# Optimization experiments

Hardware: AMD Instinct MI355X
Metric: run time of the kernel (lower is better)

The kernel has to match this reference:

```python
import jax, jax.numpy as jnp
import numpy as np

EMBED = 256
HEADS = 8
HEAD_DIM = 32
MLP_DIM = 1024
NEG = -1e9  # large negative in place of -inf so fully-deselected rows don't NaN
LN_EPS = 1e-5


def _layernorm(x, g, b):
    m = jnp.mean(x, axis=-1, keepdims=True)
    v = jnp.mean(jnp.square(x - m), axis=-1, keepdims=True)
    return (x - m) / jnp.sqrt(v + LN_EPS) * g + b


def setup_inputs() -> dict:
    key = jax.random.key(0)
    ks = jax.random.split(key, 16)
    b, s, d = 64, 360, EMBED
    sc = 0.02
    return {
        "x": jax.random.normal(ks[0], (b, s, d), dtype=jnp.float32),
        "attention_mask": jnp.zeros((b, 1, 1, s), dtype=jnp.float32),
        # TokenRouter.weight_predictor: Linear(256, 1)
        "wp_w": jax.random.normal(ks[1], (1, d), dtype=jnp.float32) * sc,
        "wp_b": jnp.zeros((1,), dtype=jnp.float32),
        # TokenRouter.aux_predictor: Linear(256,128) -> SiLU -> Linear(128,2)
        "a1_w": jax.random.normal(ks[2], (d // 2, d), dtype=jnp.float32) * sc,
        "a1_b": jnp.zeros((d // 2,), dtype=jnp.float32),
        "a2_w": jax.random.normal(ks[3], (2, d // 2), dtype=jnp.float32) * sc,
        "a2_b": jnp.zeros((2,), dtype=jnp.float32),
        # transformer block (pre-LN GPT2-style)
        "ln1_g": jnp.ones((d,), dtype=jnp.float32),
        "ln1_b": jnp.zeros((d,), dtype=jnp.float32),
        "wqkv": jax.random.normal(ks[4], (d, 3 * d), dtype=jnp.float32) * sc,
        "bqkv": jnp.zeros((3 * d,), dtype=jnp.float32),
        "wo": jax.random.normal(ks[5], (d, d), dtype=jnp.float32) * sc,
        "bo": jnp.zeros((d,), dtype=jnp.float32),
        "ln2_g": jnp.ones((d,), dtype=jnp.float32),
        "ln2_b": jnp.zeros((d,), dtype=jnp.float32),
        "w1": jax.random.normal(ks[6], (d, MLP_DIM), dtype=jnp.float32) * sc,
        "b1": jnp.zeros((MLP_DIM,), dtype=jnp.float32),
        "w2": jax.random.normal(ks[7], (MLP_DIM, d), dtype=jnp.float32) * sc,
        "b2": jnp.zeros((d,), dtype=jnp.float32),
    }


def reference(x, attention_mask, wp_w, wp_b, a1_w, a1_b, a2_w, a2_b,
              ln1_g, ln1_b, wqkv, bqkv, wo, bo, ln2_g, ln2_b, w1, b1, w2, b2):
    b, s, d = x.shape
    # --- router: per-token scalar weight ---
    weights = (x @ wp_w.T + wp_b).squeeze(-1)  # [b, s]
    # --- aux predictor selects tokens (eval path: argmax over 2 logits) ---
    h = jax.nn.silu(x @ a1_w.T + a1_b)
    aux_logits = h @ a2_w.T + a2_b            # [b, s, 2]
    sel = jnp.argmax(aux_logits, axis=-1).astype(bool)  # [b, s]
    # --- masked transformer block over the selected token subset.
    # Compacting tokens then attending == full-seq attention with deselected
    # keys masked out (LN/MLP/residual are position-wise), so vectorize:
    bias = attention_mask + jnp.where(sel, 0.0, NEG)[:, None, None, :]  # [b,1,1,s]
    hn = _layernorm(x, ln1_g, ln1_b)
    qkv = hn @ wqkv + bqkv
    q, k, v = jnp.split(qkv, 3, axis=-1)
    q = q.reshape(b, s, HEADS, HEAD_DIM)
    k = k.reshape(b, s, HEADS, HEAD_DIM)
    v = v.reshape(b, s, HEADS, HEAD_DIM)
    scores = jnp.einsum("bqhd,bkhd->bhqk", q, k) / np.sqrt(HEAD_DIM).astype(np.float32)
    scores = scores + bias                   # [b, h, s, s]
    attn = jax.nn.softmax(scores, axis=-1)
    ctx = jnp.einsum("bhqk,bkhd->bqhd", attn, v).reshape(b, s, d)
    h1 = x + (ctx @ wo + bo)
    h2n = _layernorm(h1, ln2_g, ln2_b)
    block_out = h1 + (jax.nn.gelu(h2n @ w1 + b1) @ w2 + b2)  # [b, s, d]
    # --- scatter-recombine: selected -> weighted block output, else passthrough
    out = jnp.where(sel[..., None], block_out * weights[..., None], x)
    avg_selected = jnp.sum(sel.astype(x.dtype)) / b
    return out, avg_selected
```

## Files before the change

kernel.cpp:

```cpp
#include <hip/hip_runtime.h>
#include <math.h>
#include <stdint.h>

#define TOKN 23040
#define BSZ 64
#define SEQ 360
#define DIM 256
#define NHD 8
#define HDD 32
#define MLPD 1024
#define NEGV -1e9f

typedef __attribute__((ext_vector_type(8))) short bf16x8;
typedef __attribute__((ext_vector_type(4))) float f32x4;

static __device__ __forceinline__ short f2bs(float f) {
  unsigned u = __builtin_bit_cast(unsigned, f);
  u += 0x7fffu + ((u >> 16) & 1u);
  return (short)(u >> 16);
}
static __device__ __forceinline__ float bf2f(short s) {
  unsigned u = ((unsigned)(unsigned short)s) << 16;
  return __builtin_bit_cast(float, u);
}
static __device__ __forceinline__ unsigned packbf(float a, float b) {
  return (unsigned)(unsigned short)f2bs(a) | ((unsigned)(unsigned short)f2bs(b) << 16);
}
static __device__ __forceinline__ void gl16(const short* g, short* l) {
  __builtin_amdgcn_global_load_lds(
      (const __attribute__((address_space(1))) unsigned int*)g,
      (__attribute__((address_space(3))) unsigned int*)l, 16, 0, 0);
}

__global__ __launch_bounds__(256) void mega_k(
    const float* __restrict__ x, const float* __restrict__ g,
    const float* __restrict__ b, const float* __restrict__ wpw,
    const float* __restrict__ wpb, short* __restrict__ outn,
    float* __restrict__ wout, float* __restrict__ outx,
    const float* __restrict__ a1w, const float* __restrict__ a1b,
    const float* __restrict__ a2w, const float* __restrict__ a2b,
    int* __restrict__ sel,
    const float* __restrict__ wqkv, const float* __restrict__ wo,
    const float* __restrict__ w1, const float* __restrict__ w2,
    short* __restrict__ wqkvt, short* __restrict__ wot,
    short* __restrict__ w1t, short* __restrict__ w2t) {
  __shared__ __align__(16) unsigned char smem[49152];
  int bid = blockIdx.x;
  int t = threadIdx.x;

  if (bid < 180) {
    float(*XT)[192] = (float(*)[192])smem;
    float(*WT)[192] = (float(*)[192])(smem + 24576);
    int m0 = bid * 128;
    int tx = t & 15;
    int tyy = t >> 4;
    float acc[8][8] = {};
    int rs = t >> 1, cs = (t & 1) * 16;
    int scol = (rs >> 3) * 12 + (rs & 7);
    const float* xpb = x + (size_t)(m0 + rs) * 256 + cs;
    const float* wpb_ = a1w + (size_t)rs * 256 + cs;
    for (int k0 = 0; k0 < 256; k0 += 32) {
#pragma unroll
      for (int j4 = 0; j4 < 4; j4++) {
        float4 xv4 = *(const float4*)(xpb + k0 + j4 * 4);
        float4 wv4 = *(const float4*)(wpb_ + k0 + j4 * 4);
        XT[cs + j4 * 4 + 0][scol] = xv4.x;
        XT[cs + j4 * 4 + 1][scol] = xv4.y;
        XT[cs + j4 * 4 + 2][scol] = xv4.z;
        XT[cs + j4 * 4 + 3][scol] = xv4.w;
        WT[cs + j4 * 4 + 0][scol] = wv4.x;
        WT[cs + j4 * 4 + 1][scol] = wv4.y;
        WT[cs + j4 * 4 + 2][scol] = wv4.z;
        WT[cs + j4 * 4 + 3][scol] = wv4.w;
      }
      __syncthreads();
#pragma unroll 4
      for (int kk = 0; kk < 32; kk++) {
        float4 xa = *(const float4*)&XT[kk][tyy * 12];
        float4 xb = *(const float4*)&XT[kk][tyy * 12 + 4];
        float4 wa = *(const float4*)&WT[kk][tx * 12];
        float4 wb = *(const float4*)&WT[kk][tx * 12 + 4];
        float xr[8] = {xa.x, xa.y, xa.z, xa.w, xb.x, xb.y, xb.z, xb.w};
        float wr[8] = {wa.x, wa.y, wa.z, wa.w, wb.x, wb.y, wb.z, wb.w};
#pragma unroll
        for (int i = 0; i < 8; i++)
#pragma unroll
          for (int j = 0; j < 8; j++) acc[i][j] += xr[i] * wr[j];
      }
      __syncthreads();
    }
    float b1v[8], a20[8], a21[8];
#pragma unroll
    for (int j = 0; j < 8; j++) {
      int dim = tx * 8 + j;
      b1v[j] = a1b[dim];
      a20[j] = a2w[dim];
      a21[j] = a2w[128 + dim];
    }
    float bias0 = a2b[0], bias1 = a2b[1];
#pragma unroll
    for (int i = 0; i < 8; i++) {
      float l0 = 0.f, l1 = 0.f;
#pragma unroll
      for (int j = 0; j < 8; j++) {
        float v = acc[i][j] + b1v[j];
        float h = v / (1.f + expf(-v));
        l0 += h * a20[j];
        l1 += h * a21[j];
      }
#pragma unroll
      for (int o = 1; o < 16; o <<= 1) { l0 += __shfl_xor(l0, o); l1 += __shfl_xor(l1, o); }
      if (tx == 0) sel[m0 + tyy * 8 + i] = (l1 + bias1 > l0 + bias0) ? 1 : 0;
    }
  } else if (bid < 948) {
    float(*tile)[33] = (float(*)[33])smem;
    int b2 = bid - 180;
    const float* src;
    short* dst;
    int K, N, kt, nt;
    if (b2 < 192) {
      src = wqkv; dst = wqkvt; K = 256; N = 768; kt = b2 / 24; nt = b2 % 24;
    } else if (b2 < 256) {
      int bb = b2 - 192; src = wo; dst = wot; K = 256; N = 256; kt = bb >> 3; nt = bb & 7;
    } else if (b2 < 512) {
      int bb = b2 - 256; src = w1; dst = w1t; K = 256; N = 1024; kt = bb >> 5; nt = bb & 31;
    } else {
      int bb = b2 - 512; src = w2; dst = w2t; K = 1024; N = 256; kt = bb >> 3; nt = bb & 7;
    }
    int r = t >> 3, c4 = (t & 7) * 4;
    const float4 v = *(const float4*)(src + (size_t)(kt * 32 + r) * N + nt * 32 + c4);
    tile[c4 + 0][r] = v.x;
    tile[c4 + 1][r] = v.y;
    tile[c4 + 2][r] = v.z;
    tile[c4 + 3][r] = v.w;
    __syncthreads();
    union { short s[4]; uint2 u; } o;
    o.s[0] = f2bs(tile[r][c4 + 0]);
    o.s[1] = f2bs(tile[r][c4 + 1]);
    o.s[2] = f2bs(tile[r][c4 + 2]);
    o.s[3] = f2bs(tile[r][c4 + 3]);
    *(uint2*)(dst + (size_t)(nt * 32 + r) * K + kt * 32 + c4) = o.u;
  } else {
    int tok = (bid - 948) * 4 + (t >> 6);
    int lane = t & 63;
    const float4 xv = *(const float4*)(x + (size_t)tok * DIM + lane * 4);
    *(float4*)(outx + (size_t)tok * DIM + lane * 4) = xv;
    float s = xv.x + xv.y + xv.z + xv.w;
    float s2 = xv.x * xv.x + xv.y * xv.y + xv.z * xv.z + xv.w * xv.w;
#pragma unroll
    for (int o = 1; o < 64; o <<= 1) { s += __shfl_xor(s, o); s2 += __shfl_xor(s2, o); }
    float m = s * (1.f / DIM);
    float var = fmaxf(s2 * (1.f / DIM) - m * m, 0.f);
    float rstd = rsqrtf(var + 1e-5f);
    float4 gv = *(const float4*)(g + lane * 4);
    float4 bv = *(const float4*)(b + lane * 4);
    uint2 pk;
    pk.x = packbf((xv.x - m) * rstd * gv.x + bv.x, (xv.y - m) * rstd * gv.y + bv.y);
    pk.y = packbf((xv.z - m) * rstd * gv.z + bv.z, (xv.w - m) * rstd * gv.w + bv.w);
    *(uint2*)(outn + (size_t)tok * DIM + lane * 4) = pk;
    float4 wv = *(const float4*)(wpw + lane * 4);
    float wd = xv.x * wv.x + xv.y * wv.y + xv.z * wv.z + xv.w * wv.w;
#pragma unroll
    for (int o = 1; o < 64; o <<= 1) wd += __shfl_xor(wd, o);
    if (lane == 0) wout[tok] = wd + wpb[0];
  }
}

__global__ __launch_bounds__(512) void scan_k(
    const int* __restrict__ sel, int* __restrict__ g_idx,
    int* __restrict__ startp, int* __restrict__ cntp,
    int* __restrict__ mtotp, float* __restrict__ outavg) {
  __shared__ int sc[512];
  __shared__ int red[8];
  int b = blockIdx.x, t = threadIdx.x;
  int lane = t & 63, wave = t >> 6;
  int part = 0;
  for (int i = t; i < b * SEQ; i += 512) part += sel[i];
#pragma unroll
  for (int o = 1; o < 64; o <<= 1) part += __shfl_xor(part, o);
  if (lane == 0) red[wave] = part;
  __syncthreads();
  int start = 0;
#pragma unroll
  for (int w = 0; w < 8; w++) start += red[w];
  __syncthreads();
  int flag = (t < SEQ) ? sel[b * SEQ + t] : 0;
  sc[t] = flag;
  __syncthreads();
  int val = flag;
  for (int off = 1; off < 512; off <<= 1) {
    int add = (t >= off) ? sc[t - off] : 0;
    __syncthreads();
    val += add;
    sc[t] = val;
    __syncthreads();
  }
  if (flag) g_idx[start + val - 1] = b * SEQ + t;
  if (t == 511) { startp[b] = start; cntp[b] = val; }
  if (b == 63) {
    int mt = start + sc[511];
    if (t == 0) { *mtotp = mt; outavg[0] = (float)mt / 64.0f; }
    int e = mt + 256;
    if (e > TOKN) e = TOKN;
    for (int i = mt + t; i < e; i += 512) g_idx[i] = 0;
  }
}

template <int MODE, int BN>
__global__ __launch_bounds__(256) void gemm128_k(
    const short* __restrict__ A, const short* __restrict__ Bt,
    const float* __restrict__ bias, const float* __restrict__ resf,
    const short* __restrict__ resb, const float* __restrict__ wgt,
    const int* __restrict__ g_idx, const int* __restrict__ mtotp,
    short* __restrict__ outb, float* __restrict__ outf, int Ndim, int Kdim) {
  int Mt = *mtotp;
  int m0 = blockIdx.y * 128;
  if (m0 >= Mt) return;
  __shared__ __align__(16) short As[2][128 * 32];
  __shared__ __align__(16) short Bs[2][BN * 32];
  constexpr int NJ = BN / 32;
  int n0 = blockIdx.x * BN;
  int t = threadIdx.x;
  int wave = t >> 6, lane = t & 63;
  int l15 = lane & 15, quad = lane >> 4;
  int wr = (wave >> 1) * 64, wc = (wave & 1) * (BN / 2);
  int r0 = t >> 2, c0 = (t & 3) * 8;
  long arA = (MODE == 0) ? g_idx[m0 + r0] : (m0 + r0);
  long arB = (MODE == 0) ? g_idx[m0 + 64 + r0] : (m0 + 64 + r0);
  const short* gA0 = A + arA * Kdim + c0;
  const short* gA1 = A + arB * Kdim + c0;
  const short* gB0 = Bt + (size_t)(n0 + r0) * Kdim + c0;
  const short* gB1 = Bt + (size_t)(n0 + 64 + r0) * Kdim + c0;
  int wbase = wave * 512;

  f32x4 acc[4][NJ];
#pragma unroll
  for (int i = 0; i < 4; i++)
#pragma unroll
    for (int j = 0; j < NJ; j++)
#pragma unroll
      for (int r = 0; r < 4; r++) acc[i][j][r] = 0.f;

  int nst = Kdim >> 5;
  gl16(gA0, As[0] + wbase);
  gl16(gA1, As[0] + 2048 + wbase);
  gl16(gB0, Bs[0] + wbase);
  if constexpr (BN == 128) gl16(gB1, Bs[0] + 2048 + wbase);
  __syncthreads();

  int buf = 0;
  for (int s = 0; s < nst; ++s) {
    if (s + 1 < nst) {
      int off = (s + 1) * 32;
      short* d = (buf ^ 1) ? &As[1][0] : &As[0][0];
      short* e = (buf ^ 1) ? &Bs[1][0] : &Bs[0][0];
      gl16(gA0 + off, d + wbase);
      gl16(gA1 + off, d + 2048 + wbase);
      gl16(gB0 + off, e + wbase);
      if constexpr (BN == 128) gl16(gB1 + off, e + 2048 + wbase);
    }
    const short* Ab = buf ? &As[1][0] : &As[0][0];
    const short* Bb = buf ? &Bs[1][0] : &Bs[0][0];
    bf16x8 af[4], bfr[NJ];
#pragma unroll
    for (int i = 0; i < 4; i++)
      af[i] = *(const bf16x8*)&Ab[(wr + i * 16 + l15) * 32 + quad * 8];
#pragma unroll
    for (int j = 0; j < NJ; j++)
      bfr[j] = *(const bf16x8*)&Bb[(wc + j * 16 + l15) * 32 + quad * 8];
#pragma unroll
    for (int i = 0; i < 4; i++)
#pragma unroll
      for (int j = 0; j < NJ; j++)
        acc[i][j] = __builtin_amdgcn_mfma_f32_16x16x32_bf16(af[i], bfr[j],
                                                            acc[i][j], 0, 0, 0);
    __syncthreads();
    buf ^= 1;
  }

#pragma unroll
  for (int i = 0; i < 4; i++) {
#pragma unroll
    for (int j = 0; j < NJ; j++) {
      int col = n0 + wc + j * 16 + l15;
      float bcol = bias[col];
#pragma unroll
      for (int r = 0; r < 4; r++) {
        int row = m0 + wr + i * 16 + quad * 4 + r;
        float v = acc[i][j][r] + bcol;
        size_t idx = (size_t)row * Ndim + col;
        if (MODE == 0) {
          outb[idx] = f2bs(v);
        } else if (MODE == 2) {
          float u = 0.7978845608028654f * (v + 0.044715f * v * v * v);
          float e = __expf(2.f * u);
          float th = 1.f - 2.f / (e + 1.f);
          outb[idx] = f2bs(0.5f * v * (1.f + th));
        } else {
          if (row < Mt) {
            int orig = g_idx[row];
            float o = (v + bf2f(resb[idx])) * wgt[orig];
            outf[(size_t)orig * 256 + col] = o;
          }
        }
      }
    }
  }
}

__global__ __launch_bounds__(256) void wo_ln_k(
    const short* __restrict__ A, const short* __restrict__ Bt,
    const float* __restrict__ bias, const float* __restrict__ resf,
    const float* __restrict__ g2, const float* __restrict__ b2,
    const int* __restrict__ g_idx, const int* __restrict__ mtotp,
    short* __restrict__ h1b, short* __restrict__ h2n) {
  int Mt = *mtotp;
  int m0 = blockIdx.x * 128;
  if (m0 >= Mt) return;
  __shared__ __align__(16) short As[2][128 * 32];
  __shared__ __align__(16) short Bs[2][256 * 32];
  __shared__ float ps[128][2], ps2[128][2];
  int t = threadIdx.x;
  int wave = t >> 6, lane = t & 63;
  int l15 = lane & 15, quad = lane >> 4;
  int wr = (wave >> 1) * 64, wc = (wave & 1) * 128;
  int r0 = t >> 2, c0 = (t & 3) * 8;
  const short* gA0 = A + (size_t)(m0 + r0) * 256 + c0;
  const short* gA1 = A + (size_t)(m0 + 64 + r0) * 256 + c0;
  const short* gB0 = Bt + (size_t)r0 * 256 + c0;
  int wbase = wave * 512;

  f32x4 acc[4][8];
#pragma unroll
  for (int i = 0; i < 4; i++)
#pragma unroll
    for (int j = 0; j < 8; j++)
#pragma unroll
      for (int r = 0; r < 4; r++) acc[i][j][r] = 0.f;

  gl16(gA0, As[0] + wbase);
  gl16(gA1, As[0] + 2048 + wbase);
#pragma unroll
  for (int q = 0; q < 4; q++) gl16(gB0 + (size_t)q * 64 * 256, Bs[0] + q * 2048 + wbase);
  __syncthreads();

  int buf = 0;
  for (int s = 0; s < 8; ++s) {
    if (s + 1 < 8) {
      int off = (s + 1) * 32;
      short* d = (buf ^ 1) ? &As[1][0] : &As[0][0];
      short* e = (buf ^ 1) ? &Bs[1][0] : &Bs[0][0];
      gl16(gA0 + off, d + wbase);
      gl16(gA1 + off, d + 2048 + wbase);
#pragma unroll
      for (int q = 0; q < 4; q++)
        gl16(gB0 + (size_t)q * 64 * 256 + off, e + q * 2048 + wbase);
    }
    const short* Ab = buf ? &As[1][0] : &As[0][0];
    const short* Bb = buf ? &Bs[1][0] : &Bs[0][0];
    bf16x8 af[4], bfr[8];
#pragma unroll
    for (int i = 0; i < 4; i++)
      af[i] = *(const bf16x8*)&Ab[(wr + i * 16 + l15) * 32 + quad * 8];
#pragma unroll
    for (int j = 0; j < 8; j++)
      bfr[j] = *(const bf16x8*)&Bb[(wc + j * 16 + l15) * 32 + quad * 8];
#pragma unroll
    for (int i = 0; i < 4; i++)
#pragma unroll
      for (int j = 0; j < 8; j++)
        acc[i][j] = __builtin_amdgcn_mfma_f32_16x16x32_bf16(af[i], bfr[j],
                                                            acc[i][j], 0, 0, 0);
    __syncthreads();
    buf ^= 1;
  }

  float bcol[8], gcol[8], bbcol[8];
#pragma unroll
  for (int j = 0; j < 8; j++) {
    int col = wc + j * 16 + l15;
    bcol[j] = bias[col];
    gcol[j] = g2[col];
    bbcol[j] = b2[col];
  }
  float s1v[4][4], s2v[4][4];
#pragma unroll
  for (int i = 0; i < 4; i++) {
#pragma unroll
    for (int r = 0; r < 4; r++) {
      int row = m0 + wr + i * 16 + quad * 4 + r;
      int orig = g_idx[row];
      const float* xr = resf + (size_t)orig * 256;
      float ls_ = 0.f, ls2_ = 0.f;
#pragma unroll
      for (int j = 0; j < 8; j++) {
        int col = wc + j * 16 + l15;
        float h1 = acc[i][j][r] + bcol[j] + xr[col];
        acc[i][j][r] = h1;
        h1b[(size_t)row * 256 + col] = f2bs(h1);
        ls_ += h1;
        ls2_ += h1 * h1;
      }
      s1v[i][r] = ls_;
      s2v[i][r] = ls2_;
    }
  }
#pragma unroll
  for (int i = 0; i < 4; i++)
#pragma unroll
    for (int r = 0; r < 4; r++) {
#pragma unroll
      for (int o = 1; o < 16; o <<= 1) {
        s1v[i][r] += __shfl_xor(s1v[i][r], o);
        s2v[i][r] += __shfl_xor(s2v[i][r], o);
      }
    }
  if (l15 == 0) {
#pragma unroll
    for (int i = 0; i < 4; i++)
#pragma unroll
      for (int r = 0; r < 4; r++) {
        int lr = wr + i * 16 + quad * 4 + r;
        ps[lr][wave & 1] = s1v[i][r];
        ps2[lr][wave & 1] = s2v[i][r];
      }
  }
  __syncthreads();
#pragma unroll
  for (int i = 0; i < 4; i++) {
#pragma unroll
    for (int r = 0; r < 4; r++) {
      int lr = wr + i * 16 + quad * 4 + r;
      float S = ps[lr][0] + ps[lr][1];
      float S2 = ps2[lr][0] + ps2[lr][1];
      float m = S * (1.f / 256.f);
      float var = fmaxf(S2 * (1.f / 256.f) - m * m, 0.f);
      float rstd = rsqrtf(var + 1e-5f);
      int row = m0 + lr;
#pragma unroll
      for (int j = 0; j < 8; j++) {
        int col = wc + j * 16 + l15;
        float h2 = (acc[i][j][r] - m) * rstd * gcol[j] + bbcol[j];
        h2n[(size_t)row * 256 + col] = f2bs(h2);
      }
    }
  }
}

__global__ __launch_bounds__(256) void attn_k(
    const short* __restrict__ qkv, const float* __restrict__ amask,
    const int* __restrict__ g_idx, const int* __restrict__ startp,
    const int* __restrict__ cntp, short* __restrict__ ctx) {
  __shared__ __align__(16) short VF[2 * 12 * 64 * 8];
  __shared__ __align__(16) float ls[384];
  int bh = blockIdx.x >> 1, qhalf = blockIdx.x & 1;
  int bb = bh >> 3, h = bh & 7;
  int t = threadIdx.x;
  int start = startp[bb], cnt = cntp[bb];
  size_t base = (size_t)start * 768;
  for (int i = t; i < 1536; i += 256) {
    int k = i >> 2, cg = (i & 3) * 8;
    union { int4 v; short s[8]; } u;
    if (k < cnt) {
      u.v = *(const int4*)(qkv + base + (size_t)k * 768 + 512 + h * 32 + cg);
    } else {
      u.v = make_int4(0, 0, 0, 0);
    }
    int c = k >> 5, qd = (k >> 3) & 3, j = k & 7;
#pragma unroll
    for (int jj = 0; jj < 8; jj++) {
      int d = cg + jj;
      VF[((((d >> 4) * 12 + c) * 64) + qd * 16 + (d & 15)) * 8 + j] = u.s[jj];
    }
  }
  for (int i = t; i < 384; i += 256)
    ls[i] = (i < cnt) ? amask[g_idx[start + i]] : 0.f;
  __syncthreads();

  int wave = t >> 6, lane = t & 63;
  int ql = lane & 15, quad = lane >> 4;
  int addr0 = (((quad & 1) * 2) * 16 + ql) * 4;
  int addr1 = addr0 + 64;
  bool hiq = quad >= 2;
  int nt = (cnt + 15) >> 4;
  int nc = (cnt + 31) >> 5;

  for (int qt = qhalf + 2 * wave; qt < nt; qt += 8) {
    int q0 = qt * 16, qrow = q0 + ql;
    bf16x8 qf;
#pragma unroll
    for (int j = 0; j < 8; j++) qf[j] = 0;
    if (qrow < cnt)
      qf = *(const bf16x8*)(qkv + base + (size_t)qrow * 768 + h * 32 + quad * 8);

    f32x4 o0, o1;
#pragma unroll
    for (int r = 0; r < 4; r++) { o0[r] = 0.f; o1[r] = 0.f; }
    float lsum = 0.f;

    for (int c = 0; c < nc; c++) {
      int keyA = c * 32 + ql;
      int keyB = keyA + 16;
      bf16x8 kfA, kfB;
#pragma unroll
      for (int j = 0; j < 8; j++) { kfA[j] = 0; kfB[j] = 0; }
      if (keyA < cnt)
        kfA = *(const bf16x8*)(qkv + base + (size_t)keyA * 768 + 256 + h * 32 + quad * 8);
      if (keyB < cnt)
        kfB = *(const bf16x8*)(qkv + base + (size_t)keyB * 768 + 256 + h * 32 + quad * 8);
      f32x4 sa, sb;
#pragma unroll
      for (int r = 0; r < 4; r++) { sa[r] = 0.f; sb[r] = 0.f; }
      sa = __builtin_amdgcn_mfma_f32_16x16x32_bf16(kfA, qf, sa, 0, 0, 0);
      sb = __builtin_amdgcn_mfma_f32_16x16x32_bf16(kfB, qf, sb, 0, 0, 0);
      int kbase = c * 32 + quad * 4;
      float4 la = *(const float4*)&ls[kbase];
      float4 lb = *(const float4*)&ls[kbase + 16];
      float ea0 = (kbase + 0 < cnt) ? __expf(sa[0] * 0.17677669529663687f + la.x) : 0.f;
      float ea1 = (kbase + 1 < cnt) ? __expf(sa[1] * 0.17677669529663687f + la.y) : 0.f;
      float ea2 = (kbase + 2 < cnt) ? __expf(sa[2] * 0.17677669529663687f + la.z) : 0.f;
      float ea3 = (kbase + 3 < cnt) ? __expf(sa[3] * 0.17677669529663687f + la.w) : 0.f;
      float eb0 = (kbase + 16 < cnt) ? __expf(sb[0] * 0.17677669529663687f + lb.x) : 0.f;
      float eb1 = (kbase + 17 < cnt) ? __expf(sb[1] * 0.17677669529663687f + lb.y) : 0.f;
      float eb2 = (kbase + 18 < cnt) ? __expf(sb[2] * 0.17677669529663687f + lb.z) : 0.f;
      float eb3 = (kbase + 19 < cnt) ? __expf(sb[3] * 0.17677669529663687f + lb.w) : 0.f;
      lsum += (ea0 + ea1) + (ea2 + ea3) + (eb0 + eb1) + (eb2 + eb3);
      unsigned pA0 = packbf(ea0, ea1), pA1 = packbf(ea2, ea3);
      unsigned pB0 = packbf(eb0, eb1), pB1 = packbf(eb2, eb3);
      int s00 = __builtin_amdgcn_ds_bpermute(addr0, (int)pA0);
      int s10 = __builtin_amdgcn_ds_bpermute(addr0, (int)pB0);
      int s01 = __builtin_amdgcn_ds_bpermute(addr0, (int)pA1);
      int s11 = __builtin_amdgcn_ds_bpermute(addr0, (int)pB1);
      int s02 = __builtin_amdgcn_ds_bpermute(addr1, (int)pA0);
      int s12 = __builtin_amdgcn_ds_bpermute(addr1, (int)pB0);
      int s03 = __builtin_amdgcn_ds_bpermute(addr1, (int)pA1);
      int s13 = __builtin_amdgcn_ds_bpermute(addr1, (int)pB1);
      union { int i[4]; bf16x8 v; } pf;
      pf.i[0] = hiq ? s10 : s00;
      pf.i[1] = hiq ? s11 : s01;
      pf.i[2] = hiq ? s12 : s02;
      pf.i[3] = hiq ? s13 : s03;
      bf16x8 v0 = *(const bf16x8*)&VF[(c * 64 + lane) * 8];
      bf16x8 v1 = *(const bf16x8*)&VF[((12 + c) * 64 + lane) * 8];
      o0 = __builtin_amdgcn_mfma_f32_16x16x32_bf16(v0, pf.v, o0, 0, 0, 0);
      o1 = __builtin_amdgcn_mfma_f32_16x16x32_bf16(v1, pf.v, o1, 0, 0, 0);
    }
    lsum += __shfl_xor(lsum, 16);
    lsum += __shfl_xor(lsum, 32);
    float inv = 1.f / lsum;

    if (qrow < cnt) {
      size_t cb = ((size_t)(start + qrow)) * 256 + h * 32;
      uint2 w0, w1;
      w0.x = packbf(o0[0] * inv, o0[1] * inv);
      w0.y = packbf(o0[2] * inv, o0[3] * inv);
      w1.x = packbf(o1[0] * inv, o1[1] * inv);
      w1.y = packbf(o1[2] * inv, o1[3] * inv);
      *(uint2*)(ctx + cb + quad * 4) = w0;
      *(uint2*)(ctx + cb + 16 + quad * 4) = w1;
    }
  }
}

extern "C" void kernel_launch(void* const* d_in, const int* in_sizes, int n_in,
                              void* d_out, int out_size, void* d_ws,
                              size_t ws_size, hipStream_t stream) {
  const float* x = (const float*)d_in[0];
  const float* amask = (const float*)d_in[1];
  const float* wp_w = (const float*)d_in[2];
  const float* wp_b = (const float*)d_in[3];
  const float* a1_w = (const float*)d_in[4];
  const float* a1_b = (const float*)d_in[5];
  const float* a2_w = (const float*)d_in[6];
  const float* a2_b = (const float*)d_in[7];
  const float* ln1_g = (const float*)d_in[8];
  const float* ln1_b = (const float*)d_in[9];
  const float* wqkv = (const float*)d_in[10];
  const float* bqkv = (const float*)d_in[11];
  const float* wo = (const float*)d_in[12];
  const float* bo = (const float*)d_in[13];
  const float* ln2_g = (const float*)d_in[14];
  const float* ln2_b = (const float*)d_in[15];
  const float* w1 = (const float*)d_in[16];
  const float* b1 = (const float*)d_in[17];
  const float* w2 = (const float*)d_in[18];
  const float* b2 = (const float*)d_in[19];
  float* out = (float*)d_out;

  uint8_t* p = (uint8_t*)d_ws;
  float* weightsv = (float*)p; p += (size_t)TOKN * 4;
  int* selv = (int*)p;         p += (size_t)TOKN * 4;
  int* idxlv = (int*)p;        p += (size_t)TOKN * 4;
  int* gidxv = (int*)p;        p += (size_t)TOKN * 4;
  int* cntv = (int*)p;         p += 64 * 4;
  int* startv = (int*)p;       p += 64 * 4;
  int* mtotv = (int*)p;        p += 64 * 4;
  short* wqkvt = (short*)p;    p += (size_t)768 * 256 * 2;
  short* wot = (short*)p;      p += (size_t)256 * 256 * 2;
  short* w1t = (short*)p;      p += (size_t)1024 * 256 * 2;
  short* w2t = (short*)p;      p += (size_t)256 * 1024 * 2;
  short* h1bv = (short*)p;     p += (size_t)TOKN * 256 * 2;
  short* h2nv = (short*)p;     p += (size_t)TOKN * 256 * 2;
  short* ctxv = (short*)p;     p += (size_t)TOKN * 256 * 2;
  uint8_t* R = p;
  short* xnv = (short*)R;
  short* qkvv = (short*)(R + (size_t)TOKN * 256 * 2);
  short* actv = (short*)R;
  (void)idxlv;

  mega_k<<<dim3(6708), dim3(256), 0, stream>>>(
      x, ln1_g, ln1_b, wp_w, wp_b, xnv, weightsv, out,
      a1_w, a1_b, a2_w, a2_b, selv,
      wqkv, wo, w1, w2, wqkvt, wot, w1t, w2t);
  scan_k<<<dim3(64), dim3(512), 0, stream>>>(selv, gidxv, startv, cntv, mtotv,
                                             out + (size_t)TOKN * 256);
  gemm128_k<0, 128><<<dim3(6, 180), dim3(256), 0, stream>>>(
      xnv, wqkvt, bqkv, nullptr, nullptr, nullptr, gidxv, mtotv, qkvv, nullptr,
      768, 256);
  attn_k<<<dim3(1024), dim3(256), 0, stream>>>(qkvv, amask, gidxv, startv, cntv, ctxv);
  wo_ln_k<<<dim3(180), dim3(256), 0, stream>>>(ctxv, wot, bo, x, ln2_g, ln2_b,
                                               gidxv, mtotv, h1bv, h2nv);
  gemm128_k<2, 128><<<dim3(8, 180), dim3(256), 0, stream>>>(
      h2nv, w1t, b1, nullptr, nullptr, nullptr, gidxv, mtotv, actv, nullptr,
      1024, 256);
  gemm128_k<3, 64><<<dim3(4, 180), dim3(256), 0, stream>>>(
      actv, w2t, b2, nullptr, h1bv, weightsv, gidxv, mtotv, nullptr, out, 256, 1024);
}
```

Measured before the change: 249.2 us.

## Shrink mega kernel blocks to 128 threads and retile router GEMM to 32 rows

Changes the fused prologue kernel from 256-thread to 128-thread blocks. The router GEMM now uses 32-token tiles (720 blocks instead of 180), each thread accumulating a 4x8 tile, and LDS use drops. The weight-transpose and LayerNorm sections are remapped to the smaller block. The aim is to fill more CUs with the router work, which previously ran on only 180 large blocks. In exchange, each block re-reads the full a1 weight matrix four times as often, and the block count roughly doubles.

```diff
diff --git a/kernel.cpp b/kernel.cpp
--- a/kernel.cpp
+++ b/kernel.cpp
@@ -32,7 +32,7 @@
       (__attribute__((address_space(3))) unsigned int*)l, 16, 0, 0);
 }
 
-__global__ __launch_bounds__(256) void mega_k(
+__global__ __launch_bounds__(128) void mega_k(
     const float* __restrict__ x, const float* __restrict__ g,
     const float* __restrict__ b, const float* __restrict__ wpw,
     const float* __restrict__ wpb, short* __restrict__ outn,
@@ -44,46 +44,46 @@
     const float* __restrict__ w1, const float* __restrict__ w2,
     short* __restrict__ wqkvt, short* __restrict__ wot,
     short* __restrict__ w1t, short* __restrict__ w2t) {
-  __shared__ __align__(16) unsigned char smem[49152];
+  __shared__ __align__(16) unsigned char smem[29184];
   int bid = blockIdx.x;
   int t = threadIdx.x;
 
-  if (bid < 180) {
-    float(*XT)[192] = (float(*)[192])smem;
-    float(*WT)[192] = (float(*)[192])(smem + 24576);
-    int m0 = bid * 128;
-    int tx = t & 15;
-    int tyy = t >> 4;
-    float acc[8][8] = {};
-    int rs = t >> 1, cs = (t & 1) * 16;
-    int scol = (rs >> 3) * 12 + (rs & 7);
-    const float* xpb = x + (size_t)(m0 + rs) * 256 + cs;
-    const float* wpb_ = a1w + (size_t)rs * 256 + cs;
+  if (bid < 720) {
+    float(*XT)[36] = (float(*)[36])smem;
+    float(*WT)[192] = (float(*)[192])(smem + 4608);
+    int m0 = bid * 32;
+    int tx2 = t & 15;
+    int ty2 = t >> 4;
+    float acc[4][8] = {};
+    int rr = t & 31, cb = (t >> 5) * 8;
+    const float* xp = x + (size_t)(m0 + rr) * 256 + cb;
+    const float* wp = a1w + (size_t)t * 256;
+    int wg = (t >> 3) * 12 + (t & 7);
     for (int k0 = 0; k0 < 256; k0 += 32) {
-#pragma unroll
-      for (int j4 = 0; j4 < 4; j4++) {
-        float4 xv4 = *(const float4*)(xpb + k0 + j4 * 4);
-        float4 wv4 = *(const float4*)(wpb_ + k0 + j4 * 4);
-        XT[cs + j4 * 4 + 0][scol] = xv4.x;
-        XT[cs + j4 * 4 + 1][scol] = xv4.y;
-        XT[cs + j4 * 4 + 2][scol] = xv4.z;
-        XT[cs + j4 * 4 + 3][scol] = xv4.w;
-        WT[cs + j4 * 4 + 0][scol] = wv4.x;
-        WT[cs + j4 * 4 + 1][scol] = wv4.y;
-        WT[cs + j4 * 4 + 2][scol] = wv4.z;
-        WT[cs + j4 * 4 + 3][scol] = wv4.w;
+      float4 xa = *(const float4*)(xp + k0);
+      float4 xb = *(const float4*)(xp + k0 + 4);
+      XT[cb + 0][rr] = xa.x; XT[cb + 1][rr] = xa.y;
+      XT[cb + 2][rr] = xa.z; XT[cb + 3][rr] = xa.w;
+      XT[cb + 4][rr] = xb.x; XT[cb + 5][rr] = xb.y;
+      XT[cb + 6][rr] = xb.z; XT[cb + 7][rr] = xb.w;
+#pragma unroll
+      for (int q = 0; q < 8; q++) {
+        float4 wv = *(const float4*)(wp + k0 + q * 4);
+        WT[q * 4 + 0][wg] = wv.x;
+        WT[q * 4 + 1][wg] = wv.y;
+        WT[q * 4 + 2][wg] = wv.z;
+        WT[q * 4 + 3][wg] = wv.w;
       }
       __syncthreads();
 #pragma unroll 4
       for (int kk = 0; kk < 32; kk++) {
-        float4 xa = *(const float4*)&XT[kk][tyy * 12];
-        float4 xb = *(const float4*)&XT[kk][tyy * 12 + 4];
-        float4 wa = *(const float4*)&WT[kk][tx * 12];
-        float4 wb = *(const float4*)&WT[kk][tx * 12 + 4];
-        float xr[8] = {xa.x, xa.y, xa.z, xa.w, xb.x, xb.y, xb.z, xb.w};
+        float4 xv4 = *(const float4*)&XT[kk][ty2 * 4];
+        float4 wa = *(const float4*)&WT[kk][tx2 * 12];
+        float4 wb = *(const float4*)&WT[kk][tx2 * 12 + 4];
+        float xr[4] = {xv4.x, xv4.y, xv4.z, xv4.w};
         float wr[8] = {wa.x, wa.y, wa.z, wa.w, wb.x, wb.y, wb.z, wb.w};
 #pragma unroll
-        for (int i = 0; i < 8; i++)
+        for (int i = 0; i < 4; i++)
 #pragma unroll
           for (int j = 0; j < 8; j++) acc[i][j] += xr[i] * wr[j];
       }
@@ -92,14 +92,14 @@
     float b1v[8], a20[8], a21[8];
 #pragma unroll
     for (int j = 0; j < 8; j++) {
-      int dim = tx * 8 + j;
+      int dim = tx2 * 8 + j;
       b1v[j] = a1b[dim];
       a20[j] = a2w[dim];
       a21[j] = a2w[128 + dim];
     }
     float bias0 = a2b[0], bias1 = a2b[1];
 #pragma unroll
-    for (int i = 0; i < 8; i++) {
+    for (int i = 0; i < 4; i++) {
       float l0 = 0.f, l1 = 0.f;
 #pragma unroll
       for (int j = 0; j < 8; j++) {
@@ -110,11 +110,11 @@
       }
 #pragma unroll
       for (int o = 1; o < 16; o <<= 1) { l0 += __shfl_xor(l0, o); l1 += __shfl_xor(l1, o); }
-      if (tx == 0) sel[m0 + tyy * 8 + i] = (l1 + bias1 > l0 + bias0) ? 1 : 0;
-    }
-  } else if (bid < 948) {
+      if (tx2 == 0) sel[m0 + ty2 * 4 + i] = (l1 + bias1 > l0 + bias0) ? 1 : 0;
+    }
+  } else if (bid < 1488) {
     float(*tile)[33] = (float(*)[33])smem;
-    int b2 = bid - 180;
+    int b2 = bid - 720;
     const float* src;
     short* dst;
     int K, N, kt, nt;
@@ -127,21 +127,27 @@
     } else {
       int bb = b2 - 512; src = w2; dst = w2t; K = 1024; N = 256; kt = bb >> 3; nt = bb & 7;
     }
-    int r = t >> 3, c4 = (t & 7) * 4;
-    const float4 v = *(const float4*)(src + (size_t)(kt * 32 + r) * N + nt * 32 + c4);
-    tile[c4 + 0][r] = v.x;
-    tile[c4 + 1][r] = v.y;
-    tile[c4 + 2][r] = v.z;
-    tile[c4 + 3][r] = v.w;
+    int r = t >> 2, c8 = (t & 3) * 8;
+#pragma unroll
+    for (int h2 = 0; h2 < 2; h2++) {
+      const float4 v = *(const float4*)(src + (size_t)(kt * 32 + r) * N + nt * 32 + c8 + h2 * 4);
+      tile[c8 + h2 * 4 + 0][r] = v.x;
+      tile[c8 + h2 * 4 + 1][r] = v.y;
+      tile[c8 + h2 * 4 + 2][r] = v.z;
+      tile[c8 + h2 * 4 + 3][r] = v.w;
+    }
     __syncthreads();
-    union { short s[4]; uint2 u; } o;
-    o.s[0] = f2bs(tile[r][c4 + 0]);
-    o.s[1] = f2bs(tile[r][c4 + 1]);
-    o.s[2] = f2bs(tile[r][c4 + 2]);
-    o.s[3] = f2bs(tile[r][c4 + 3]);
-    *(uint2*)(dst + (size_t)(nt * 32 + r) * K + kt * 32 + c4) = o.u;
+#pragma unroll
+    for (int h2 = 0; h2 < 2; h2++) {
+      union { short s[4]; uint2 u; } o;
+      o.s[0] = f2bs(tile[r][c8 + h2 * 4 + 0]);
+      o.s[1] = f2bs(tile[r][c8 + h2 * 4 + 1]);
+      o.s[2] = f2bs(tile[r][c8 + h2 * 4 + 2]);
+      o.s[3] = f2bs(tile[r][c8 + h2 * 4 + 3]);
+      *(uint2*)(dst + (size_t)(nt * 32 + r) * K + kt * 32 + c8 + h2 * 4) = o.u;
+    }
   } else {
-    int tok = (bid - 948) * 4 + (t >> 6);
+    int tok = (bid - 1488) * 2 + (t >> 6);
     int lane = t & 63;
     const float4 xv = *(const float4*)(x + (size_t)tok * DIM + lane * 4);
     *(float4*)(outx + (size_t)tok * DIM + lane * 4) = xv;
@@ -608,7 +614,7 @@
   short* actv = (short*)R;
   (void)idxlv;
 
-  mega_k<<<dim3(6708), dim3(256), 0, stream>>>(
+  mega_k<<<dim3(13008), dim3(128), 0, stream>>>(
       x, ln1_g, ln1_b, wp_w, wp_b, xnv, weightsv, out,
       a1_w, a1_b, a2_w, a2_b, selv,
       wqkv, wo, w1, w2, wqkvt, wot, w1t, w2t);
```

New measurement: 253.5 us. Within noise of the previous version (+1.8%).
